# Kernel optimization log

Hardware: AMD Instinct MI355X
Metric: run time of the kernel (lower is better)

## Reference

```python
import jax, jax.numpy as jnp
import numpy as np

WIND = 5
PYR_W = (1.0, 0.5, 0.25, 0.125)
# torch bicubic (a=-0.75), scale 0.5, align_corners=False: frac offset is always 0.5
# -> fixed separable 4-tap kernel, taps at src indices 2i-1..2i+2 (edge-clamped)
BICUBIC_TAPS = (-0.09375, 0.59375, 0.59375, -0.09375)


def _windows(x):
    # x: (B,1,H,W) -> (B,25,H,W); window index k = di*5+dj, value = zero-padded x[h+di, w+dj]
    B, _, H, W = x.shape
    p = jnp.pad(x[:, 0], ((0, 0), (2, 2), (2, 2)))
    return jnp.stack([p[:, di:di + H, dj:dj + W]
                      for di in range(WIND) for dj in range(WIND)], axis=1)


def _down2_axis(a, axis):
    pad = [(0, 0)] * a.ndim
    pad[axis] = (1, 2)  # taps 2i-1..2i+2, replicate border like torch
    p = jnp.pad(a, pad, mode='edge')
    Ho = a.shape[axis] // 2
    out = None
    for k, w in enumerate(BICUBIC_TAPS):
        idx = [slice(None)] * a.ndim
        idx[axis] = slice(k, k + 2 * Ho, 2)
        t = w * p[tuple(idx)]
        out = t if out is None else out + t
    return out


def _down2(x):
    # bicubic downsample by 2 on (B,C,H,W), matching F.interpolate(scale_factor=0.5, mode='bicubic')
    return _down2_axis(_down2_axis(x, 2), 3)


def _level_loss(fake, hdr, window, rw):
    # window: (1,25,1,1) (all-ones, not normalized in the bilateral branch)
    weights_map = window * rw                                   # (B,25,H,W)
    wsum = jnp.sum(weights_map, axis=1, keepdims=True)          # (B,1,H,W)
    fake_bf = jnp.sum(_windows(fake) * weights_map, axis=1, keepdims=True) / wsum
    hdr_bf = jnp.sum(_windows(hdr) * weights_map, axis=1, keepdims=True) / wsum
    return jnp.mean((fake_bf - jax.lax.stop_gradient(hdr_bf)) ** 2)


def setup_inputs() -> dict:
    key = jax.random.key(0)
    ks = jax.random.split(key, 8)
    B, H, W = 8, 512, 512
    inp = {
        'fake': jax.random.uniform(ks[0], (B, 1, H, W), dtype=jnp.float32),
        'hdr_input': jax.random.uniform(ks[1], (B, 1, H, W), dtype=jnp.float32),
        'window': jnp.ones((1, WIND * WIND, 1, 1), dtype=jnp.float32),
    }
    for i in range(4):
        s = H >> i
        inp[f'r_weights_{i}'] = jax.random.uniform(ks[2 + i], (B, WIND * WIND, s, s), dtype=jnp.float32)
    return inp


def reference(fake, hdr_input, window, r_weights_0, r_weights_1, r_weights_2, r_weights_3):
    rws = (r_weights_0, r_weights_1, r_weights_2, r_weights_3)
    total = jnp.float32(0.0)
    f, h = fake, hdr_input
    for pw, rw in zip(PYR_W, rws):
        total = total + pw * _level_loss(f, h, window, rw)
        f = _down2(f)
        h = _down2(h)
    return total
```

## Files before the change

kernel.cpp:

```cpp
#include <hip/hip_runtime.h>
#include <hip/hip_bf16.h>

template <int PX, bool WD>
__global__ __launch_bounds__(256) void loss_kernel(
    const float* __restrict__ F0, const float* __restrict__ H0,
    const float* __restrict__ window, const float* __restrict__ rw,
    double* __restrict__ slots, int S, float scale,
    float* __restrict__ fdown, float* __restrict__ hdown)
{
    constexpr int TW = PX * 64;
    __shared__ float sf[8][TW + 4];
    __shared__ float sh[8][TW + 4];
    __shared__ float swin[25];
    __shared__ float wred[4];

    const int tx = threadIdx.x, ty = threadIdx.y;
    const int tid = ty * 64 + tx;
    if (tid < 25) swin[tid] = window[tid];

    const int bx0 = blockIdx.x * TW, by0 = blockIdx.y * 4, b = blockIdx.z;
    const float* F  = F0 + (size_t)b * S * S;
    const float* Hp = H0 + (size_t)b * S * S;

    for (int i = tid; i < 8 * (TW + 4); i += 256) {
        const int r = i / (TW + 4), c = i % (TW + 4);
        const int y = by0 + r - 2, x = bx0 + c - 2;
        float fv = 0.f, hv = 0.f;
        if ((unsigned)y < (unsigned)S && (unsigned)x < (unsigned)S) {
            const size_t id = (size_t)y * S + x;
            fv = F[id]; hv = Hp[id];
        }
        sf[r][c] = fv; sh[r][c] = hv;
    }
    __syncthreads();

    const int x0 = bx0 + PX * tx, y = by0 + ty;
    const size_t ks = (size_t)S * S;
    const float* rwp = rw + (size_t)b * 25 * ks + (size_t)y * S + x0;

    float wsum[PX], fs[PX], hs[PX];
#pragma unroll
    for (int p = 0; p < PX; ++p) { wsum[p] = 0.f; fs[p] = 0.f; hs[p] = 0.f; }

#pragma unroll
    for (int di = 0; di < 5; ++di) {
        float f6[PX + 4], h6[PX + 4];
        if constexpr (PX == 2) {
            const float2* pf = (const float2*)&sf[ty + di][2 * tx];
            const float2* ph = (const float2*)&sh[ty + di][2 * tx];
            float2 a = pf[0], bb = pf[1], cc = pf[2];
            f6[0] = a.x; f6[1] = a.y; f6[2] = bb.x; f6[3] = bb.y; f6[4] = cc.x; f6[5] = cc.y;
            float2 d = ph[0], e = ph[1], g = ph[2];
            h6[0] = d.x; h6[1] = d.y; h6[2] = e.x; h6[3] = e.y; h6[4] = g.x; h6[5] = g.y;
        } else {
#pragma unroll
            for (int j = 0; j < 5; ++j) {
                f6[j] = sf[ty + di][tx + j];
                h6[j] = sh[ty + di][tx + j];
            }
        }
#pragma unroll
        for (int dj = 0; dj < 5; ++dj) {
            const int k = di * 5 + dj;
            float rv[PX];
            if constexpr (PX == 2) {
                const float2 t = *(const float2*)(rwp + (size_t)k * ks);
                rv[0] = t.x; rv[1] = t.y;
            } else {
                rv[0] = rwp[(size_t)k * ks];
            }
#pragma unroll
            for (int p = 0; p < PX; ++p) {
                const float wm = swin[k] * rv[p];
                wsum[p] += wm;
                fs[p] = fmaf(wm, f6[dj + p], fs[p]);
                hs[p] = fmaf(wm, h6[dj + p], hs[p]);
            }
        }
    }
    float v = 0.f;
#pragma unroll
    for (int p = 0; p < PX; ++p) {
        const float d = (fs[p] - hs[p]) / wsum[p];
        v = fmaf(d, d, v);
    }

#pragma unroll
    for (int off = 32; off > 0; off >>= 1) v += __shfl_down(v, off, 64);
    if ((tid & 63) == 0) wred[tid >> 6] = v;

    if constexpr (WD) {
        const int Sh = S >> 1;
        if (tid < 128 * PX) {
            const int img = tid >= 64 * PX;
            const int t2 = tid & (64 * PX - 1);
            const int r = t2 / (PX * 32), c = t2 % (PX * 32);
            const int y1 = (by0 >> 1) + r, x1 = (bx0 >> 1) + c;
            const float wt[4] = {-0.09375f, 0.59375f, 0.59375f, -0.09375f};
            float (*s)[TW + 4] = img ? sh : sf;
            int lc[4];
#pragma unroll
            for (int kx = 0; kx < 4; ++kx) {
                int gx = bx0 + 2 * c - 1 + kx;
                lc[kx] = min(max(gx, 0), S - 1) - bx0 + 2;
            }
            float acc = 0.f;
#pragma unroll
            for (int ky = 0; ky < 4; ++ky) {
                int gy = by0 + 2 * r - 1 + ky;
                const int lr = min(max(gy, 0), S - 1) - by0 + 2;
                const float rs = wt[0] * (s[lr][lc[0]] + s[lr][lc[3]])
                               + wt[1] * (s[lr][lc[1]] + s[lr][lc[2]]);
                acc = fmaf(wt[ky], rs, acc);
            }
            float* dst = img ? hdown : fdown;
            dst[((size_t)b * Sh + y1) * Sh + x1] = acc;
        }
    }

    __syncthreads();
    if (tid == 0) {
        const float sB = wred[0] + wred[1] + wred[2] + wred[3];
        const unsigned lin = blockIdx.x + gridDim.x * (blockIdx.y + gridDim.y * blockIdx.z);
        slots[lin] = (double)sB * (double)scale;
    }
}

__global__ void finalize_kernel(const double* __restrict__ slots, float* __restrict__ out, int n)
{
    __shared__ double wred[4];
    const int t = threadIdx.x;
    double s = 0.0;
    for (int i = t; i < n; i += 256) s += slots[i];
#pragma unroll
    for (int off = 32; off > 0; off >>= 1) s += __shfl_down(s, off, 64);
    if ((t & 63) == 0) wred[t >> 6] = s;
    __syncthreads();
    if (t == 0) out[0] = (float)(wred[0] + wred[1] + wred[2] + wred[3]);
}

extern "C" void kernel_launch(void* const* d_in, const int* in_sizes, int n_in,
                              void* d_out, int out_size, void* d_ws, size_t ws_size,
                              hipStream_t stream)
{
    const float* fake   = (const float*)d_in[0];
    const float* hdr    = (const float*)d_in[1];
    const float* window = (const float*)d_in[2];
    const float* rw0    = (const float*)d_in[3];
    const float* rw1    = (const float*)d_in[4];
    const float* rw2    = (const float*)d_in[5];
    const float* rw3    = (const float*)d_in[6];
    float* out = (float*)d_out;

    const int B = 8;
    char* ws = (char*)d_ws;
    double* slots = (double*)ws;
    float* f1 = (float*)(ws + 65536);
    const size_t n1 = (size_t)B * 256 * 256;
    float* h1 = f1 + n1;
    float* f2 = h1 + n1;
    const size_t n2 = (size_t)B * 128 * 128;
    float* h2 = f2 + n2;
    float* f3 = h2 + n2;
    const size_t n3 = (size_t)B * 64 * 64;
    float* h3 = f3 + n3;

    const dim3 blk(64, 4);

    loss_kernel<2, true><<<dim3(4, 128, B), blk, 0, stream>>>(
        fake, hdr, window, rw0, slots, 512, 1.0f / (8.f * 512.f * 512.f), f1, h1);
    loss_kernel<2, true><<<dim3(2, 64, B), blk, 0, stream>>>(
        f1, h1, window, rw1, slots + 4096, 256, 0.5f / (8.f * 256.f * 256.f), f2, h2);
    loss_kernel<2, true><<<dim3(1, 32, B), blk, 0, stream>>>(
        f2, h2, window, rw2, slots + 5120, 128, 0.25f / (8.f * 128.f * 128.f), f3, h3);
    loss_kernel<1, false><<<dim3(1, 16, B), blk, 0, stream>>>(
        f3, h3, window, rw3, slots + 5376, 64, 0.125f / (8.f * 64.f * 64.f),
        nullptr, nullptr);

    finalize_kernel<<<1, 256, 0, stream>>>(slots, out, 5504);
}
```

Before: 73.77 us.

## Widen per-thread tiles to 4 pixels and fuse last two pyramid levels

Levels 0 and 1 now have each thread handle 4 pixels with float4 loads of the r_weights and the shared tiles, halving the block count and widening the memory accesses. Levels 2 and 3 are merged into one launch. Level-3 blocks recompute the 64x64 bicubic downsample of level 2 in shared memory, so no intermediate is written and one launch is removed. The tradeoff is redundant downsample work and a larger shared-memory footprint in the tail kernel, plus fewer, larger blocks for the top levels, which reduces occupancy.

Measured after the change: 70.25 us. 1.05x faster.

```diff
diff --git a/kernel.cpp b/kernel.cpp
--- a/kernel.cpp
+++ b/kernel.cpp
@@ -1,26 +1,32 @@
 #include <hip/hip_runtime.h>
 #include <hip/hip_bf16.h>
 
-template <int PX, bool WD>
-__global__ __launch_bounds__(256) void loss_kernel(
+#define WT0 (-0.09375f)
+#define WT1 (0.59375f)
+
+template <int S>
+__global__ __launch_bounds__(256) void loss_down_kernel(
     const float* __restrict__ F0, const float* __restrict__ H0,
-    const float* __restrict__ window, const float* __restrict__ rw,
-    double* __restrict__ slots, int S, float scale,
-    float* __restrict__ fdown, float* __restrict__ hdown)
+    const float* __restrict__ window, const float* __restrict__ RW,
+    double* __restrict__ slots, float scale,
+    float* __restrict__ fd, float* __restrict__ hd)
 {
-    constexpr int TW = PX * 64;
-    __shared__ float sf[8][TW + 4];
-    __shared__ float sh[8][TW + 4];
+    constexpr int TW = 256;
+    __shared__ __align__(16) float sf[8][TW + 4];
+    __shared__ __align__(16) float sh[8][TW + 4];
     __shared__ float swin[25];
     __shared__ float wred[4];
 
-    const int tx = threadIdx.x, ty = threadIdx.y;
-    const int tid = ty * 64 + tx;
+    const int tid = threadIdx.x;
+    const int tx = tid & 63, ty = tid >> 6;
     if (tid < 25) swin[tid] = window[tid];
 
-    const int bx0 = blockIdx.x * TW, by0 = blockIdx.y * 4, b = blockIdx.z;
-    const float* F  = F0 + (size_t)b * S * S;
-    const float* Hp = H0 + (size_t)b * S * S;
+    const int bx0 = blockIdx.x * TW;
+    const int by0 = blockIdx.y * 4;
+    const int b   = blockIdx.z;
+
+    const float* Fb = F0 + (size_t)b * S * S;
+    const float* Hb = H0 + (size_t)b * S * S;
 
     for (int i = tid; i < 8 * (TW + 4); i += 256) {
         const int r = i / (TW + 4), c = i % (TW + 4);
@@ -28,93 +34,85 @@
         float fv = 0.f, hv = 0.f;
         if ((unsigned)y < (unsigned)S && (unsigned)x < (unsigned)S) {
             const size_t id = (size_t)y * S + x;
-            fv = F[id]; hv = Hp[id];
+            fv = Fb[id]; hv = Hb[id];
         }
         sf[r][c] = fv; sh[r][c] = hv;
     }
     __syncthreads();
 
-    const int x0 = bx0 + PX * tx, y = by0 + ty;
+    const int x0 = bx0 + 4 * tx, y = by0 + ty;
     const size_t ks = (size_t)S * S;
-    const float* rwp = rw + (size_t)b * 25 * ks + (size_t)y * S + x0;
-
-    float wsum[PX], fs[PX], hs[PX];
-#pragma unroll
-    for (int p = 0; p < PX; ++p) { wsum[p] = 0.f; fs[p] = 0.f; hs[p] = 0.f; }
-
+    const float* rwp = RW + (size_t)b * 25 * ks + (size_t)y * S + x0;
+
+    float wsum[4] = {0.f, 0.f, 0.f, 0.f};
+    float fs[4]   = {0.f, 0.f, 0.f, 0.f};
+    float hs[4]   = {0.f, 0.f, 0.f, 0.f};
 #pragma unroll
     for (int di = 0; di < 5; ++di) {
-        float f6[PX + 4], h6[PX + 4];
-        if constexpr (PX == 2) {
-            const float2* pf = (const float2*)&sf[ty + di][2 * tx];
-            const float2* ph = (const float2*)&sh[ty + di][2 * tx];
-            float2 a = pf[0], bb = pf[1], cc = pf[2];
-            f6[0] = a.x; f6[1] = a.y; f6[2] = bb.x; f6[3] = bb.y; f6[4] = cc.x; f6[5] = cc.y;
-            float2 d = ph[0], e = ph[1], g = ph[2];
-            h6[0] = d.x; h6[1] = d.y; h6[2] = e.x; h6[3] = e.y; h6[4] = g.x; h6[5] = g.y;
-        } else {
-#pragma unroll
-            for (int j = 0; j < 5; ++j) {
-                f6[j] = sf[ty + di][tx + j];
-                h6[j] = sh[ty + di][tx + j];
-            }
+        float f9[9], h9[9];
+        {
+            const float4* pf = (const float4*)&sf[ty + di][4 * tx];
+            const float4 a0 = pf[0], a1 = pf[1];
+            f9[0]=a0.x; f9[1]=a0.y; f9[2]=a0.z; f9[3]=a0.w;
+            f9[4]=a1.x; f9[5]=a1.y; f9[6]=a1.z; f9[7]=a1.w;
+            f9[8]=sf[ty + di][4 * tx + 8];
+            const float4* ph = (const float4*)&sh[ty + di][4 * tx];
+            const float4 b0 = ph[0], b1 = ph[1];
+            h9[0]=b0.x; h9[1]=b0.y; h9[2]=b0.z; h9[3]=b0.w;
+            h9[4]=b1.x; h9[5]=b1.y; h9[6]=b1.z; h9[7]=b1.w;
+            h9[8]=sh[ty + di][4 * tx + 8];
         }
 #pragma unroll
         for (int dj = 0; dj < 5; ++dj) {
             const int k = di * 5 + dj;
-            float rv[PX];
-            if constexpr (PX == 2) {
-                const float2 t = *(const float2*)(rwp + (size_t)k * ks);
-                rv[0] = t.x; rv[1] = t.y;
-            } else {
-                rv[0] = rwp[(size_t)k * ks];
-            }
-#pragma unroll
-            for (int p = 0; p < PX; ++p) {
-                const float wm = swin[k] * rv[p];
-                wsum[p] += wm;
-                fs[p] = fmaf(wm, f6[dj + p], fs[p]);
-                hs[p] = fmaf(wm, h6[dj + p], hs[p]);
-            }
+            const float4 rv = *(const float4*)(rwp + (size_t)k * ks);
+            const float w0 = swin[k] * rv.x;
+            const float w1 = swin[k] * rv.y;
+            const float w2 = swin[k] * rv.z;
+            const float w3 = swin[k] * rv.w;
+            wsum[0] += w0; wsum[1] += w1; wsum[2] += w2; wsum[3] += w3;
+            fs[0] = fmaf(w0, f9[dj + 0], fs[0]);
+            fs[1] = fmaf(w1, f9[dj + 1], fs[1]);
+            fs[2] = fmaf(w2, f9[dj + 2], fs[2]);
+            fs[3] = fmaf(w3, f9[dj + 3], fs[3]);
+            hs[0] = fmaf(w0, h9[dj + 0], hs[0]);
+            hs[1] = fmaf(w1, h9[dj + 1], hs[1]);
+            hs[2] = fmaf(w2, h9[dj + 2], hs[2]);
+            hs[3] = fmaf(w3, h9[dj + 3], hs[3]);
         }
     }
     float v = 0.f;
 #pragma unroll
-    for (int p = 0; p < PX; ++p) {
+    for (int p = 0; p < 4; ++p) {
         const float d = (fs[p] - hs[p]) / wsum[p];
         v = fmaf(d, d, v);
     }
-
 #pragma unroll
     for (int off = 32; off > 0; off >>= 1) v += __shfl_down(v, off, 64);
     if ((tid & 63) == 0) wred[tid >> 6] = v;
 
-    if constexpr (WD) {
-        const int Sh = S >> 1;
-        if (tid < 128 * PX) {
-            const int img = tid >= 64 * PX;
-            const int t2 = tid & (64 * PX - 1);
-            const int r = t2 / (PX * 32), c = t2 % (PX * 32);
-            const int y1 = (by0 >> 1) + r, x1 = (bx0 >> 1) + c;
-            const float wt[4] = {-0.09375f, 0.59375f, 0.59375f, -0.09375f};
+    {
+        constexpr int Sh = S / 2;
+        const float wt[4] = {WT0, WT1, WT1, WT0};
+        for (int i = tid; i < 512; i += 256) {
+            const int img = i >> 8, t2 = i & 255;
+            const int r = t2 >> 7, c = t2 & 127;
+            const int g1y = (by0 >> 1) + r, g1x = (bx0 >> 1) + c;
             float (*s)[TW + 4] = img ? sh : sf;
             int lc[4];
 #pragma unroll
-            for (int kx = 0; kx < 4; ++kx) {
-                int gx = bx0 + 2 * c - 1 + kx;
-                lc[kx] = min(max(gx, 0), S - 1) - bx0 + 2;
-            }
+            for (int kx = 0; kx < 4; ++kx)
+                lc[kx] = min(max(bx0 + 2 * c - 1 + kx, 0), S - 1) - bx0 + 2;
             float acc = 0.f;
 #pragma unroll
             for (int ky = 0; ky < 4; ++ky) {
-                int gy = by0 + 2 * r - 1 + ky;
-                const int lr = min(max(gy, 0), S - 1) - by0 + 2;
-                const float rs = wt[0] * (s[lr][lc[0]] + s[lr][lc[3]])
-                               + wt[1] * (s[lr][lc[1]] + s[lr][lc[2]]);
+                const int lr = min(max(by0 + 2 * r - 1 + ky, 0), S - 1) - by0 + 2;
+                const float rs = WT0 * (s[lr][lc[0]] + s[lr][lc[3]])
+                               + WT1 * (s[lr][lc[1]] + s[lr][lc[2]]);
                 acc = fmaf(wt[ky], rs, acc);
             }
-            float* dst = img ? hdown : fdown;
-            dst[((size_t)b * Sh + y1) * Sh + x1] = acc;
+            float* dst = img ? hd : fd;
+            dst[((size_t)b * Sh + g1y) * Sh + g1x] = acc;
         }
     }
 
@@ -126,17 +124,149 @@
     }
 }
 
+__global__ __launch_bounds__(256) void loss_tail_kernel(
+    const float* __restrict__ window,
+    const float* __restrict__ rw2, const float* __restrict__ rw3,
+    const float* __restrict__ f2, const float* __restrict__ h2,
+    double* __restrict__ slots)
+{
+    __shared__ float s2f[8][132];
+    __shared__ float s2h[8][132];
+    __shared__ float p2[2][18][128];
+    __shared__ float l3[2][8][68];
+    __shared__ float swin[25];
+    __shared__ float wred[4];
+
+    const int tid = threadIdx.x;
+    const int tx = tid & 63, ty = tid >> 6;
+    if (tid < 25) swin[tid] = window[tid];
+    const int lin = blockIdx.x;
+
+    float v = 0.f;
+    float scale;
+
+    if (lin < 256) {
+        const int b = lin >> 5, by0 = (lin & 31) * 4;
+        const float* Fb = f2 + (size_t)b * 128 * 128;
+        const float* Hb = h2 + (size_t)b * 128 * 128;
+        for (int i = tid; i < 8 * 132; i += 256) {
+            const int r = i / 132, c = i % 132;
+            const int y = by0 + r - 2, x = c - 2;
+            float fv = 0.f, hv = 0.f;
+            if ((unsigned)y < 128u && (unsigned)x < 128u) {
+                const size_t id = (size_t)y * 128 + x;
+                fv = Fb[id]; hv = Hb[id];
+            }
+            s2f[r][c] = fv; s2h[r][c] = hv;
+        }
+        __syncthreads();
+
+        const int x0 = 2 * tx, y = by0 + ty;
+        const size_t ks = 128 * 128;
+        const float* rwp = rw2 + (size_t)b * 25 * ks + (size_t)y * 128 + x0;
+        float wsum[2] = {0.f, 0.f}, fs[2] = {0.f, 0.f}, hs[2] = {0.f, 0.f};
+#pragma unroll
+        for (int di = 0; di < 5; ++di) {
+            float f6[6], h6[6];
+            const float2* pf = (const float2*)&s2f[ty + di][2 * tx];
+            const float2 a0 = pf[0], a1 = pf[1], a2 = pf[2];
+            f6[0]=a0.x; f6[1]=a0.y; f6[2]=a1.x; f6[3]=a1.y; f6[4]=a2.x; f6[5]=a2.y;
+            const float2* ph = (const float2*)&s2h[ty + di][2 * tx];
+            const float2 b0 = ph[0], b1 = ph[1], b2 = ph[2];
+            h6[0]=b0.x; h6[1]=b0.y; h6[2]=b1.x; h6[3]=b1.y; h6[4]=b2.x; h6[5]=b2.y;
+#pragma unroll
+            for (int dj = 0; dj < 5; ++dj) {
+                const int k = di * 5 + dj;
+                const float2 rv = *(const float2*)(rwp + (size_t)k * ks);
+                const float w0 = swin[k] * rv.x;
+                const float w1 = swin[k] * rv.y;
+                wsum[0] += w0; wsum[1] += w1;
+                fs[0] = fmaf(w0, f6[dj + 0], fs[0]);
+                fs[1] = fmaf(w1, f6[dj + 1], fs[1]);
+                hs[0] = fmaf(w0, h6[dj + 0], hs[0]);
+                hs[1] = fmaf(w1, h6[dj + 1], hs[1]);
+            }
+        }
+        const float d0 = (fs[0] - hs[0]) / wsum[0];
+        const float d1 = (fs[1] - hs[1]) / wsum[1];
+        v = fmaf(d0, d0, d1 * d1);
+        scale = 0.25f / (8.f * 128.f * 128.f);
+    } else {
+        const int t = lin - 256;
+        const int b = t >> 4, by0 = (t & 15) * 4;
+        const int fr0 = 2 * by0 - 5;
+        for (int i = tid; i < 2 * 18 * 128; i += 256) {
+            const int img = i / 2304, j = i % 2304;
+            const int r = j >> 7, c = j & 127;
+            const int gy = min(max(fr0 + r, 0), 127);
+            p2[img][r][c] = (img ? h2 : f2)[((size_t)b * 128 + gy) * 128 + c];
+        }
+        __syncthreads();
+        const float wt[4] = {WT0, WT1, WT1, WT0};
+        for (int i = tid; i < 2 * 8 * 68; i += 256) {
+            const int img = i / 544, j = i % 544;
+            const int r = j / 68, c = j % 68;
+            const int gy = by0 - 2 + r, gx = c - 2;
+            float a = 0.f;
+            if ((unsigned)gy < 64u && (unsigned)gx < 64u) {
+                int ry[4], cx[4];
+#pragma unroll
+                for (int k = 0; k < 4; ++k) {
+                    ry[k] = min(max(2 * gy - 1 + k, 0), 127) - fr0;
+                    cx[k] = min(max(2 * gx - 1 + k, 0), 127);
+                }
+#pragma unroll
+                for (int ky = 0; ky < 4; ++ky) {
+                    const float* row = p2[img][ry[ky]];
+                    const float rs = WT0 * (row[cx[0]] + row[cx[3]])
+                                   + WT1 * (row[cx[1]] + row[cx[2]]);
+                    a = fmaf(wt[ky], rs, a);
+                }
+            }
+            l3[img][r][c] = a;
+        }
+        __syncthreads();
+
+        const size_t ks = 64 * 64;
+        const float* rwp = rw3 + (size_t)b * 25 * ks + (size_t)(by0 + ty) * 64 + tx;
+        float wsum = 0.f, fs = 0.f, hs = 0.f;
+#pragma unroll
+        for (int di = 0; di < 5; ++di) {
+#pragma unroll
+            for (int dj = 0; dj < 5; ++dj) {
+                const int k = di * 5 + dj;
+                const float wm = swin[k] * rwp[(size_t)k * ks];
+                wsum += wm;
+                fs = fmaf(wm, l3[0][ty + di][tx + dj], fs);
+                hs = fmaf(wm, l3[1][ty + di][tx + dj], hs);
+            }
+        }
+        const float d = (fs - hs) / wsum;
+        v = d * d;
+        scale = 0.125f / (8.f * 64.f * 64.f);
+    }
+
+#pragma unroll
+    for (int off = 32; off > 0; off >>= 1) v += __shfl_down(v, off, 64);
+    if ((tid & 63) == 0) wred[tid >> 6] = v;
+    __syncthreads();
+    if (tid == 0) {
+        const float sB = wred[0] + wred[1] + wred[2] + wred[3];
+        slots[lin] = (double)sB * (double)scale;
+    }
+}
+
 __global__ void finalize_kernel(const double* __restrict__ slots, float* __restrict__ out, int n)
 {
-    __shared__ double wred[4];
+    __shared__ double dred[4];
     const int t = threadIdx.x;
     double s = 0.0;
     for (int i = t; i < n; i += 256) s += slots[i];
 #pragma unroll
     for (int off = 32; off > 0; off >>= 1) s += __shfl_down(s, off, 64);
-    if ((t & 63) == 0) wred[t >> 6] = s;
+    if ((t & 63) == 0) dred[t >> 6] = s;
     __syncthreads();
-    if (t == 0) out[0] = (float)(wred[0] + wred[1] + wred[2] + wred[3]);
+    if (t == 0) out[0] = (float)(dred[0] + dred[1] + dred[2] + dred[3]);
 }
 
 extern "C" void kernel_launch(void* const* d_in, const int* in_sizes, int n_in,
@@ -155,27 +285,21 @@
     const int B = 8;
     char* ws = (char*)d_ws;
     double* slots = (double*)ws;
-    float* f1 = (float*)(ws + 65536);
+    float* f1 = (float*)(ws + 32768);
     const size_t n1 = (size_t)B * 256 * 256;
     float* h1 = f1 + n1;
     float* f2 = h1 + n1;
     const size_t n2 = (size_t)B * 128 * 128;
     float* h2 = f2 + n2;
-    float* f3 = h2 + n2;
-    const size_t n3 = (size_t)B * 64 * 64;
-    float* h3 = f3 + n3;
-
-    const dim3 blk(64, 4);
-
-    loss_kernel<2, true><<<dim3(4, 128, B), blk, 0, stream>>>(
-        fake, hdr, window, rw0, slots, 512, 1.0f / (8.f * 512.f * 512.f), f1, h1);
-    loss_kernel<2, true><<<dim3(2, 64, B), blk, 0, stream>>>(
-        f1, h1, window, rw1, slots + 4096, 256, 0.5f / (8.f * 256.f * 256.f), f2, h2);
-    loss_kernel<2, true><<<dim3(1, 32, B), blk, 0, stream>>>(
-        f2, h2, window, rw2, slots + 5120, 128, 0.25f / (8.f * 128.f * 128.f), f3, h3);
-    loss_kernel<1, false><<<dim3(1, 16, B), blk, 0, stream>>>(
-        f3, h3, window, rw3, slots + 5376, 64, 0.125f / (8.f * 64.f * 64.f),
-        nullptr, nullptr);
-
-    finalize_kernel<<<1, 256, 0, stream>>>(slots, out, 5504);
+
+    loss_down_kernel<512><<<dim3(2, 128, B), 256, 0, stream>>>(
+        fake, hdr, window, rw0, slots, 1.0f / (8.f * 512.f * 512.f), f1, h1);
+
+    loss_down_kernel<256><<<dim3(1, 64, B), 256, 0, stream>>>(
+        f1, h1, window, rw1, slots + 2048, 0.5f / (8.f * 256.f * 256.f), f2, h2);
+
+    loss_tail_kernel<<<dim3(384), 256, 0, stream>>>(
+        window, rw2, rw3, f2, h2, slots + 2560);
+
+    finalize_kernel<<<1, 256, 0, stream>>>(slots, out, 2944);
 }
```

## Fuse pyramid downsampling into one kernel and batch coarser levels

Applied to the files above, without the earlier changes.

Replaces four dependent per-level launches with two. The first kernel computes the level-0 loss in 4-pixel-wide tiles and, in separate blocks, builds all three downsampled pyramid levels directly from the full-resolution input using haloed shared-memory tiles. The second kernel computes the losses for levels 1-3 together in one grid. This removes the serial dependency chain and the launch gaps between small kernels, at the cost of recomputing halo regions and loading extra input per downsample block.

After: 72.97 us. Within noise of the previous version (-1.1%).

```diff
diff --git a/kernel.cpp b/kernel.cpp
--- a/kernel.cpp
+++ b/kernel.cpp
@@ -1,42 +1,36 @@
 #include <hip/hip_runtime.h>
 #include <hip/hip_bf16.h>
 
-template <int PX, bool WD>
-__global__ __launch_bounds__(256) void loss_kernel(
-    const float* __restrict__ F0, const float* __restrict__ H0,
-    const float* __restrict__ window, const float* __restrict__ rw,
-    double* __restrict__ slots, int S, float scale,
-    float* __restrict__ fdown, float* __restrict__ hdown)
-{
-    constexpr int TW = PX * 64;
-    __shared__ float sf[8][TW + 4];
-    __shared__ float sh[8][TW + 4];
-    __shared__ float swin[25];
-    __shared__ float wred[4];
-
-    const int tx = threadIdx.x, ty = threadIdx.y;
-    const int tid = ty * 64 + tx;
-    if (tid < 25) swin[tid] = window[tid];
-
-    const int bx0 = blockIdx.x * TW, by0 = blockIdx.y * 4, b = blockIdx.z;
-    const float* F  = F0 + (size_t)b * S * S;
-    const float* Hp = H0 + (size_t)b * S * S;
-
-    for (int i = tid; i < 8 * (TW + 4); i += 256) {
-        const int r = i / (TW + 4), c = i % (TW + 4);
+#define WT0 (-0.09375f)
+#define WT1 (0.59375f)
+
+template <int S, int PX>
+__device__ __forceinline__ float bilat_tile(
+    const float* __restrict__ Fb, const float* __restrict__ Hb,
+    const float* __restrict__ rwB,
+    float* __restrict__ sf, float* __restrict__ sh,
+    const float* __restrict__ swin,
+    int bx0, int by0, int tid)
+{
+    constexpr int TW = 64 * PX;
+    constexpr int LW = TW + 4;
+    const int tx = tid & 63, ty = tid >> 6;
+
+    for (int i = tid; i < 8 * LW; i += 256) {
+        const int r = i / LW, c = i % LW;
         const int y = by0 + r - 2, x = bx0 + c - 2;
         float fv = 0.f, hv = 0.f;
         if ((unsigned)y < (unsigned)S && (unsigned)x < (unsigned)S) {
             const size_t id = (size_t)y * S + x;
-            fv = F[id]; hv = Hp[id];
-        }
-        sf[r][c] = fv; sh[r][c] = hv;
+            fv = Fb[id]; hv = Hb[id];
+        }
+        sf[r * LW + c] = fv; sh[r * LW + c] = hv;
     }
     __syncthreads();
 
     const int x0 = bx0 + PX * tx, y = by0 + ty;
     const size_t ks = (size_t)S * S;
-    const float* rwp = rw + (size_t)b * 25 * ks + (size_t)y * S + x0;
+    const float* rwp = rwB + (size_t)y * S + x0;
 
     float wsum[PX], fs[PX], hs[PX];
 #pragma unroll
@@ -44,28 +38,22 @@
 
 #pragma unroll
     for (int di = 0; di < 5; ++di) {
-        float f6[PX + 4], h6[PX + 4];
-        if constexpr (PX == 2) {
-            const float2* pf = (const float2*)&sf[ty + di][2 * tx];
-            const float2* ph = (const float2*)&sh[ty + di][2 * tx];
-            float2 a = pf[0], bb = pf[1], cc = pf[2];
-            f6[0] = a.x; f6[1] = a.y; f6[2] = bb.x; f6[3] = bb.y; f6[4] = cc.x; f6[5] = cc.y;
-            float2 d = ph[0], e = ph[1], g = ph[2];
-            h6[0] = d.x; h6[1] = d.y; h6[2] = e.x; h6[3] = e.y; h6[4] = g.x; h6[5] = g.y;
-        } else {
-#pragma unroll
-            for (int j = 0; j < 5; ++j) {
-                f6[j] = sf[ty + di][tx + j];
-                h6[j] = sh[ty + di][tx + j];
-            }
+        float f9[PX + 4], h9[PX + 4];
+#pragma unroll
+        for (int j = 0; j < PX + 4; ++j) {
+            f9[j] = sf[(ty + di) * LW + PX * tx + j];
+            h9[j] = sh[(ty + di) * LW + PX * tx + j];
         }
 #pragma unroll
         for (int dj = 0; dj < 5; ++dj) {
             const int k = di * 5 + dj;
             float rv[PX];
-            if constexpr (PX == 2) {
-                const float2 t = *(const float2*)(rwp + (size_t)k * ks);
-                rv[0] = t.x; rv[1] = t.y;
+            if constexpr (PX == 4) {
+                const float4 t4 = *(const float4*)(rwp + (size_t)k * ks);
+                rv[0] = t4.x; rv[1] = t4.y; rv[2] = t4.z; rv[3] = t4.w;
+            } else if constexpr (PX == 2) {
+                const float2 t2 = *(const float2*)(rwp + (size_t)k * ks);
+                rv[0] = t2.x; rv[1] = t2.y;
             } else {
                 rv[0] = rwp[(size_t)k * ks];
             }
@@ -73,8 +61,8 @@
             for (int p = 0; p < PX; ++p) {
                 const float wm = swin[k] * rv[p];
                 wsum[p] += wm;
-                fs[p] = fmaf(wm, f6[dj + p], fs[p]);
-                hs[p] = fmaf(wm, h6[dj + p], hs[p]);
+                fs[p] = fmaf(wm, f9[dj + p], fs[p]);
+                hs[p] = fmaf(wm, h9[dj + p], hs[p]);
             }
         }
     }
@@ -84,59 +72,199 @@
         const float d = (fs[p] - hs[p]) / wsum[p];
         v = fmaf(d, d, v);
     }
-
+    return v;
+}
+
+__device__ __forceinline__ void reduce_and_store(
+    float v, float scale, int tid, float* wred, double* slot)
+{
 #pragma unroll
     for (int off = 32; off > 0; off >>= 1) v += __shfl_down(v, off, 64);
     if ((tid & 63) == 0) wred[tid >> 6] = v;
-
-    if constexpr (WD) {
-        const int Sh = S >> 1;
-        if (tid < 128 * PX) {
-            const int img = tid >= 64 * PX;
-            const int t2 = tid & (64 * PX - 1);
-            const int r = t2 / (PX * 32), c = t2 % (PX * 32);
-            const int y1 = (by0 >> 1) + r, x1 = (bx0 >> 1) + c;
-            const float wt[4] = {-0.09375f, 0.59375f, 0.59375f, -0.09375f};
-            float (*s)[TW + 4] = img ? sh : sf;
-            int lc[4];
-#pragma unroll
-            for (int kx = 0; kx < 4; ++kx) {
-                int gx = bx0 + 2 * c - 1 + kx;
-                lc[kx] = min(max(gx, 0), S - 1) - bx0 + 2;
-            }
-            float acc = 0.f;
-#pragma unroll
-            for (int ky = 0; ky < 4; ++ky) {
-                int gy = by0 + 2 * r - 1 + ky;
-                const int lr = min(max(gy, 0), S - 1) - by0 + 2;
-                const float rs = wt[0] * (s[lr][lc[0]] + s[lr][lc[3]])
-                               + wt[1] * (s[lr][lc[1]] + s[lr][lc[2]]);
-                acc = fmaf(wt[ky], rs, acc);
-            }
-            float* dst = img ? hdown : fdown;
-            dst[((size_t)b * Sh + y1) * Sh + x1] = acc;
-        }
-    }
-
     __syncthreads();
     if (tid == 0) {
-        const float sB = wred[0] + wred[1] + wred[2] + wred[3];
-        const unsigned lin = blockIdx.x + gridDim.x * (blockIdx.y + gridDim.y * blockIdx.z);
-        slots[lin] = (double)sB * (double)scale;
-    }
+        const float s = wred[0] + wred[1] + wred[2] + wred[3];
+        *slot = (double)s * (double)scale;
+    }
+}
+
+__global__ __launch_bounds__(256) void k1_kernel(
+    const float* __restrict__ fake, const float* __restrict__ hdr,
+    const float* __restrict__ window, const float* __restrict__ rw0,
+    double* __restrict__ slots,
+    float* __restrict__ f1, float* __restrict__ h1,
+    float* __restrict__ f2, float* __restrict__ h2,
+    float* __restrict__ f3, float* __restrict__ h3)
+{
+    __shared__ float smem[6400];
+    __shared__ float swin[25];
+    __shared__ float wred[4];
+
+    const int tid = threadIdx.x;
+    if (tid < 25) swin[tid] = window[tid];
+    const int lin = blockIdx.x;
+
+    if (lin < 2048) {
+        const int b = lin >> 8, t = lin & 255;
+        const int by0 = (t >> 1) * 4, bx0 = (t & 1) * 256;
+        const float v = bilat_tile<512, 4>(
+            fake + (size_t)b * 512 * 512, hdr + (size_t)b * 512 * 512,
+            rw0 + (size_t)b * 25 * 512 * 512,
+            smem, smem + 2080, swin, bx0, by0, tid);
+        reduce_and_store(v, 1.0f / (8.f * 512.f * 512.f), tid, wred, &slots[lin]);
+        return;
+    }
+
+    const int p = lin - 2048;
+    const int b = p >> 8, q = p & 255;
+    const int Y = q >> 4, X = q & 15;
+    float* s0  = smem;
+    float* l1t = smem + 5000;
+    float* l2t = smem + 6152;
+    const float* srcF = fake + (size_t)b * 512 * 512;
+    const float* srcH = hdr  + (size_t)b * 512 * 512;
+    const float wt[4] = {WT0, WT1, WT1, WT0};
+
+    const int r0 = 32 * Y - 7, c0 = 32 * X - 7;
+    for (int i = tid; i < 2 * 50 * 50; i += 256) {
+        const int img = i / 2500, j = i % 2500;
+        const int r = j / 50, c = j % 50;
+        const int gy = min(max(r0 + r, 0), 511);
+        const int gx = min(max(c0 + c, 0), 511);
+        s0[i] = (img ? srcH : srcF)[(size_t)gy * 512 + gx];
+    }
+    __syncthreads();
+
+    const int r1 = 16 * Y - 3, c1 = 16 * X - 3;
+    for (int i = tid; i < 2 * 24 * 24; i += 256) {
+        const int img = i / 576, j = i % 576;
+        const int r = j / 24, c = j % 24;
+        const int g1y = min(max(r1 + r, 0), 255);
+        const int g1x = min(max(c1 + c, 0), 255);
+        int sy[4], sx[4];
+#pragma unroll
+        for (int k = 0; k < 4; ++k) {
+            sy[k] = min(max(2 * g1y - 1 + k, 0), 511) - r0;
+            sx[k] = min(max(2 * g1x - 1 + k, 0), 511) - c0;
+        }
+        float a = 0.f;
+#pragma unroll
+        for (int ky = 0; ky < 4; ++ky) {
+            const float* row = s0 + img * 2500 + sy[ky] * 50;
+            const float rs = WT0 * (row[sx[0]] + row[sx[3]]) + WT1 * (row[sx[1]] + row[sx[2]]);
+            a = fmaf(wt[ky], rs, a);
+        }
+        l1t[i] = a;
+        if (r >= 3 && r < 19 && c >= 3 && c < 19) {
+            float* dst = img ? h1 : f1;
+            dst[((size_t)b * 256 + (r1 + r)) * 256 + (c1 + c)] = a;
+        }
+    }
+    __syncthreads();
+
+    const int r2 = 8 * Y - 1, c2 = 8 * X - 1;
+    for (int i = tid; i < 2 * 11 * 11; i += 256) {
+        const int img = i / 121, j = i % 121;
+        const int r = j / 11, c = j % 11;
+        const int g2y = min(max(r2 + r, 0), 127);
+        const int g2x = min(max(c2 + c, 0), 127);
+        int sy[4], sx[4];
+#pragma unroll
+        for (int k = 0; k < 4; ++k) {
+            sy[k] = min(max(2 * g2y - 1 + k, 0), 255) - r1;
+            sx[k] = min(max(2 * g2x - 1 + k, 0), 255) - c1;
+        }
+        float a = 0.f;
+#pragma unroll
+        for (int ky = 0; ky < 4; ++ky) {
+            const float* row = l1t + img * 576 + sy[ky] * 24;
+            const float rs = WT0 * (row[sx[0]] + row[sx[3]]) + WT1 * (row[sx[1]] + row[sx[2]]);
+            a = fmaf(wt[ky], rs, a);
+        }
+        l2t[i] = a;
+        if (r >= 1 && r < 9 && c >= 1 && c < 9) {
+            float* dst = img ? h2 : f2;
+            dst[((size_t)b * 128 + (r2 + r)) * 128 + (c2 + c)] = a;
+        }
+    }
+    __syncthreads();
+
+    for (int i = tid; i < 2 * 4 * 4; i += 256) {
+        const int img = i / 16, j = i % 16;
+        const int r = j / 4, c = j % 4;
+        const int g3y = 4 * Y + r, g3x = 4 * X + c;
+        int sy[4], sx[4];
+#pragma unroll
+        for (int k = 0; k < 4; ++k) {
+            sy[k] = min(max(2 * g3y - 1 + k, 0), 127) - r2;
+            sx[k] = min(max(2 * g3x - 1 + k, 0), 127) - c2;
+        }
+        float a = 0.f;
+#pragma unroll
+        for (int ky = 0; ky < 4; ++ky) {
+            const float* row = l2t + img * 121 + sy[ky] * 11;
+            const float rs = WT0 * (row[sx[0]] + row[sx[3]]) + WT1 * (row[sx[1]] + row[sx[2]]);
+            a = fmaf(wt[ky], rs, a);
+        }
+        float* dst = img ? h3 : f3;
+        dst[((size_t)b * 64 + g3y) * 64 + g3x] = a;
+    }
+}
+
+__global__ __launch_bounds__(256) void k2_kernel(
+    const float* __restrict__ window,
+    const float* __restrict__ rw1, const float* __restrict__ rw2,
+    const float* __restrict__ rw3,
+    const float* __restrict__ f1, const float* __restrict__ h1,
+    const float* __restrict__ f2, const float* __restrict__ h2,
+    const float* __restrict__ f3, const float* __restrict__ h3,
+    double* __restrict__ slots)
+{
+    __shared__ float smem[4160];
+    __shared__ float swin[25];
+    __shared__ float wred[4];
+
+    const int tid = threadIdx.x;
+    if (tid < 25) swin[tid] = window[tid];
+    const int lin = blockIdx.x;
+
+    float v, scale;
+    if (lin < 512) {
+        const int b = lin >> 6, by0 = (lin & 63) * 4;
+        v = bilat_tile<256, 4>(
+            f1 + (size_t)b * 65536, h1 + (size_t)b * 65536,
+            rw1 + (size_t)b * 25 * 65536,
+            smem, smem + 2080, swin, 0, by0, tid);
+        scale = 0.5f / (8.f * 256.f * 256.f);
+    } else if (lin < 768) {
+        const int t = lin - 512, b = t >> 5, by0 = (t & 31) * 4;
+        v = bilat_tile<128, 2>(
+            f2 + (size_t)b * 16384, h2 + (size_t)b * 16384,
+            rw2 + (size_t)b * 25 * 16384,
+            smem, smem + 1056, swin, 0, by0, tid);
+        scale = 0.25f / (8.f * 128.f * 128.f);
+    } else {
+        const int t = lin - 768, b = t >> 4, by0 = (t & 15) * 4;
+        v = bilat_tile<64, 1>(
+            f3 + (size_t)b * 4096, h3 + (size_t)b * 4096,
+            rw3 + (size_t)b * 25 * 4096,
+            smem, smem + 544, swin, 0, by0, tid);
+        scale = 0.125f / (8.f * 64.f * 64.f);
+    }
+    reduce_and_store(v, scale, tid, wred, &slots[2048 + lin]);
 }
 
 __global__ void finalize_kernel(const double* __restrict__ slots, float* __restrict__ out, int n)
 {
-    __shared__ double wred[4];
+    __shared__ double dred[4];
     const int t = threadIdx.x;
     double s = 0.0;
     for (int i = t; i < n; i += 256) s += slots[i];
 #pragma unroll
     for (int off = 32; off > 0; off >>= 1) s += __shfl_down(s, off, 64);
-    if ((t & 63) == 0) wred[t >> 6] = s;
-    __syncthreads();
-    if (t == 0) out[0] = (float)(wred[0] + wred[1] + wred[2] + wred[3]);
+    if ((t & 63) == 0) dred[t >> 6] = s;
+    __syncthreads();
+    if (t == 0) out[0] = (float)(dred[0] + dred[1] + dred[2] + dred[3]);
 }
 
 extern "C" void kernel_launch(void* const* d_in, const int* in_sizes, int n_in,
@@ -155,7 +283,7 @@
     const int B = 8;
     char* ws = (char*)d_ws;
     double* slots = (double*)ws;
-    float* f1 = (float*)(ws + 65536);
+    float* f1 = (float*)(ws + 32768);
     const size_t n1 = (size_t)B * 256 * 256;
     float* h1 = f1 + n1;
     float* f2 = h1 + n1;
@@ -165,17 +293,11 @@
     const size_t n3 = (size_t)B * 64 * 64;
     float* h3 = f3 + n3;
 
-    const dim3 blk(64, 4);
-
-    loss_kernel<2, true><<<dim3(4, 128, B), blk, 0, stream>>>(
-        fake, hdr, window, rw0, slots, 512, 1.0f / (8.f * 512.f * 512.f), f1, h1);
-    loss_kernel<2, true><<<dim3(2, 64, B), blk, 0, stream>>>(
-        f1, h1, window, rw1, slots + 4096, 256, 0.5f / (8.f * 256.f * 256.f), f2, h2);
-    loss_kernel<2, true><<<dim3(1, 32, B), blk, 0, stream>>>(
-        f2, h2, window, rw2, slots + 5120, 128, 0.25f / (8.f * 128.f * 128.f), f3, h3);
-    loss_kernel<1, false><<<dim3(1, 16, B), blk, 0, stream>>>(
-        f3, h3, window, rw3, slots + 5376, 64, 0.125f / (8.f * 64.f * 64.f),
-        nullptr, nullptr);
-
-    finalize_kernel<<<1, 256, 0, stream>>>(slots, out, 5504);
-}
+    k1_kernel<<<dim3(4096), 256, 0, stream>>>(
+        fake, hdr, window, rw0, slots, f1, h1, f2, h2, f3, h3);
+
+    k2_kernel<<<dim3(896), 256, 0, stream>>>(
+        window, rw1, rw2, rw3, f1, h1, f2, h2, f3, h3, slots);
+
+    finalize_kernel<<<1, 256, 0, stream>>>(slots, out, 2944);
+}
```
